# Kernel tuning notes

Measured on AMD Instinct MI355X. Metric: run time of the kernel, lower is better.

Reference implementation:

```python
import jax, jax.numpy as jnp
import numpy as np

N_LEAVES = 256
N_CLASSES = 512
BATCH = 131072


def setup_inputs() -> dict:
    key = jax.random.key(0)
    k1, k2 = jax.random.split(key)
    # opinions: concatenated leaf class distributions [n_leaves, n_classes]
    opinions = jax.random.normal(k1, (N_LEAVES, N_CLASSES), dtype=jnp.float32)
    # weights: concatenated per-leaf path probabilities [batch, n_leaves]
    weights = jax.random.uniform(k2, (BATCH, N_LEAVES), dtype=jnp.float32)
    return {"opinions": opinions, "weights": weights}


def reference(opinions, weights):
    # argmax over leaves per example, then gather that leaf's opinion row.
    # Equivalent to tf: elems = argmax(weights, axis=1); map_fn(lambda x: opinions[x], elems)
    idx = jnp.argmax(weights, axis=1)            # [batch]
    return jnp.take(opinions, idx, axis=0)       # [batch, n_classes]
```

## Files before the change

### kernel.cpp

```cpp
#include <hip/hip_runtime.h>

#define N_LEAVES  256
#define N_CLASSES 512

__global__ __launch_bounds__(256) void OutputLayer_41961830482215_kernel(
    const float* __restrict__ opinions,
    const float* __restrict__ weights,
    float* __restrict__ out,
    int batch)
{
    const int wave = threadIdx.x >> 6;
    const int lane = threadIdx.x & 63;
    const long long row = (long long)blockIdx.x * 4 + wave;
    if (row >= batch) return;

    const float4 w = *reinterpret_cast<const float4*>(weights + row * N_LEAVES + lane * 4);
    float best = w.x;
    int   bidx = lane * 4;
    if (w.y > best) { best = w.y; bidx = lane * 4 + 1; }
    if (w.z > best) { best = w.z; bidx = lane * 4 + 2; }
    if (w.w > best) { best = w.w; bidx = lane * 4 + 3; }

    #pragma unroll
    for (int off = 32; off >= 1; off >>= 1) {
        const float ov = __shfl_xor(best, off);
        const int   oi = __shfl_xor(bidx, off);
        if (ov > best || (ov == best && oi < bidx)) { best = ov; bidx = oi; }
    }

    const float4* __restrict__ src =
        reinterpret_cast<const float4*>(opinions + (long long)bidx * N_CLASSES);
    float4* __restrict__ dst =
        reinterpret_cast<float4*>(out + row * N_CLASSES);
    dst[lane]      = src[lane];
    dst[lane + 64] = src[lane + 64];
}

extern "C" void kernel_launch(void* const* d_in, const int* in_sizes, int n_in,
                              void* d_out, int out_size, void* d_ws, size_t ws_size,
                              hipStream_t stream) {
    const float* opinions = (const float*)d_in[0];
    const float* weights  = (const float*)d_in[1];
    float* out = (float*)d_out;
    const int batch = in_sizes[1] / N_LEAVES;
    const int blocks = (batch + 3) / 4;
    OutputLayer_41961830482215_kernel<<<blocks, 256, 0, stream>>>(
        opinions, weights, out, batch);
}
```

Baseline: 79.18 us.

## Split argmax and gather into two kernels via workspace index buffer

Splits the fused argmax+gather kernel into an argmax kernel that writes per-row indices to the workspace and a gather kernel that copies opinion rows. The fused kernel is kept as a fallback when the workspace is too small. The aim is to separate the read-heavy and write-heavy phases so each streams more cleanly. In exchange it adds a second launch and an extra round trip of the index array through memory.

```diff
diff --git a/kernel.cpp b/kernel.cpp
--- a/kernel.cpp
+++ b/kernel.cpp
@@ -3,10 +3,11 @@
 #define N_LEAVES  256
 #define N_CLASSES 512
 
-__global__ __launch_bounds__(256) void OutputLayer_41961830482215_kernel(
-    const float* __restrict__ opinions,
+typedef float f32x4 __attribute__((ext_vector_type(4)));
+
+__global__ __launch_bounds__(256) void argmax_rows_kernel(
     const float* __restrict__ weights,
-    float* __restrict__ out,
+    int* __restrict__ idx,
     int batch)
 {
     const int wave = threadIdx.x >> 6;
@@ -14,7 +15,7 @@
     const long long row = (long long)blockIdx.x * 4 + wave;
     if (row >= batch) return;
 
-    const float4 w = *reinterpret_cast<const float4*>(weights + row * N_LEAVES + lane * 4);
+    const f32x4 w = *(reinterpret_cast<const f32x4*>(weights + row * N_LEAVES) + lane);
     float best = w.x;
     int   bidx = lane * 4;
     if (w.y > best) { best = w.y; bidx = lane * 4 + 1; }
@@ -27,11 +28,54 @@
         const int   oi = __shfl_xor(bidx, off);
         if (ov > best || (ov == best && oi < bidx)) { best = ov; bidx = oi; }
     }
+    if (lane == 0) idx[row] = bidx;
+}
 
-    const float4* __restrict__ src =
-        reinterpret_cast<const float4*>(opinions + (long long)bidx * N_CLASSES);
-    float4* __restrict__ dst =
-        reinterpret_cast<float4*>(out + row * N_CLASSES);
+__global__ __launch_bounds__(256) void gather_rows_kernel(
+    const float* __restrict__ opinions,
+    const int* __restrict__ idx,
+    float* __restrict__ out,
+    int batch)
+{
+    const int wave = threadIdx.x >> 6;
+    const int lane = threadIdx.x & 63;
+    const long long row = (long long)blockIdx.x * 4 + wave;
+    if (row >= batch) return;
+
+    const int b = idx[row];
+    const f32x4* __restrict__ src =
+        reinterpret_cast<const f32x4*>(opinions + (long long)b * N_CLASSES);
+    f32x4* __restrict__ dst = reinterpret_cast<f32x4*>(out + row * N_CLASSES);
+    dst[lane]      = src[lane];
+    dst[lane + 64] = src[lane + 64];
+}
+
+__global__ __launch_bounds__(256) void fused_kernel(
+    const float* __restrict__ opinions,
+    const float* __restrict__ weights,
+    float* __restrict__ out,
+    int batch)
+{
+    const int wave = threadIdx.x >> 6;
+    const int lane = threadIdx.x & 63;
+    const long long row = (long long)blockIdx.x * 4 + wave;
+    if (row >= batch) return;
+
+    const f32x4 w = *(reinterpret_cast<const f32x4*>(weights + row * N_LEAVES) + lane);
+    float best = w.x;
+    int   bidx = lane * 4;
+    if (w.y > best) { best = w.y; bidx = lane * 4 + 1; }
+    if (w.z > best) { best = w.z; bidx = lane * 4 + 2; }
+    if (w.w > best) { best = w.w; bidx = lane * 4 + 3; }
+    #pragma unroll
+    for (int off = 32; off >= 1; off >>= 1) {
+        const float ov = __shfl_xor(best, off);
+        const int   oi = __shfl_xor(bidx, off);
+        if (ov > best || (ov == best && oi < bidx)) { best = ov; bidx = oi; }
+    }
+    const f32x4* __restrict__ src =
+        reinterpret_cast<const f32x4*>(opinions + (long long)bidx * N_CLASSES);
+    f32x4* __restrict__ dst = reinterpret_cast<f32x4*>(out + row * N_CLASSES);
     dst[lane]      = src[lane];
     dst[lane + 64] = src[lane + 64];
 }
@@ -44,6 +88,12 @@
     float* out = (float*)d_out;
     const int batch = in_sizes[1] / N_LEAVES;
     const int blocks = (batch + 3) / 4;
-    OutputLayer_41961830482215_kernel<<<blocks, 256, 0, stream>>>(
-        opinions, weights, out, batch);
+
+    if (ws_size >= (size_t)batch * sizeof(int)) {
+        int* idx = (int*)d_ws;
+        argmax_rows_kernel<<<blocks, 256, 0, stream>>>(weights, idx, batch);
+        gather_rows_kernel<<<blocks, 256, 0, stream>>>(opinions, idx, out, batch);
+    } else {
+        fused_kernel<<<blocks, 256, 0, stream>>>(opinions, weights, out, batch);
+    }
 }
```

New measurement: 86.89 us. 1.1x slower.

## Use persistent grid-stride loop with next-row prefetch and nontemporal loads/stores

Applied to the files above, without the earlier changes.

Replaces the one-row-per-wave launch with a fixed grid of 2048 blocks. Each wave loops over rows with a grid stride and prefetches the next row's weights before reducing the current one. Weight loads and output stores use nontemporal hints to avoid polluting the cache, while opinion rows stay cached. This aims to hide load latency and cut launch and scheduling overhead. The risk is lower occupancy-driven parallelism on a kernel that is bandwidth-bound.

```diff
diff --git a/kernel.cpp b/kernel.cpp
--- a/kernel.cpp
+++ b/kernel.cpp
@@ -2,6 +2,8 @@
 
 #define N_LEAVES  256
 #define N_CLASSES 512
+
+typedef float f32x4 __attribute__((ext_vector_type(4)));
 
 __global__ __launch_bounds__(256) void OutputLayer_41961830482215_kernel(
     const float* __restrict__ opinions,
@@ -11,29 +13,45 @@
 {
     const int wave = threadIdx.x >> 6;
     const int lane = threadIdx.x & 63;
-    const long long row = (long long)blockIdx.x * 4 + wave;
+    const long long W   = (long long)gridDim.x * 4;
+    const long long gid = (long long)blockIdx.x * 4 + wave;
+
+    long long row = gid;
     if (row >= batch) return;
 
-    const float4 w = *reinterpret_cast<const float4*>(weights + row * N_LEAVES + lane * 4);
-    float best = w.x;
-    int   bidx = lane * 4;
-    if (w.y > best) { best = w.y; bidx = lane * 4 + 1; }
-    if (w.z > best) { best = w.z; bidx = lane * 4 + 2; }
-    if (w.w > best) { best = w.w; bidx = lane * 4 + 3; }
+    f32x4 w_next = __builtin_nontemporal_load(
+        reinterpret_cast<const f32x4*>(weights + row * N_LEAVES) + lane);
 
-    #pragma unroll
-    for (int off = 32; off >= 1; off >>= 1) {
-        const float ov = __shfl_xor(best, off);
-        const int   oi = __shfl_xor(bidx, off);
-        if (ov > best || (ov == best && oi < bidx)) { best = ov; bidx = oi; }
+    while (row < batch) {
+        const f32x4 w = w_next;
+        const long long nrow = row + W;
+        if (nrow < batch) {
+            w_next = __builtin_nontemporal_load(
+                reinterpret_cast<const f32x4*>(weights + nrow * N_LEAVES) + lane);
+        }
+
+        float best = w.x;
+        int   bidx = lane * 4;
+        if (w.y > best) { best = w.y; bidx = lane * 4 + 1; }
+        if (w.z > best) { best = w.z; bidx = lane * 4 + 2; }
+        if (w.w > best) { best = w.w; bidx = lane * 4 + 3; }
+        #pragma unroll
+        for (int off = 32; off >= 1; off >>= 1) {
+            const float ov = __shfl_xor(best, off);
+            const int   oi = __shfl_xor(bidx, off);
+            if (ov > best || (ov == best && oi < bidx)) { best = ov; bidx = oi; }
+        }
+
+        const f32x4* __restrict__ src =
+            reinterpret_cast<const f32x4*>(opinions + (long long)bidx * N_CLASSES);
+        const f32x4 lo = src[lane];
+        const f32x4 hi = src[lane + 64];
+        f32x4* dst = reinterpret_cast<f32x4*>(out + row * N_CLASSES);
+        __builtin_nontemporal_store(lo, dst + lane);
+        __builtin_nontemporal_store(hi, dst + lane + 64);
+
+        row = nrow;
     }
-
-    const float4* __restrict__ src =
-        reinterpret_cast<const float4*>(opinions + (long long)bidx * N_CLASSES);
-    float4* __restrict__ dst =
-        reinterpret_cast<float4*>(out + row * N_CLASSES);
-    dst[lane]      = src[lane];
-    dst[lane + 64] = src[lane + 64];
 }
 
 extern "C" void kernel_launch(void* const* d_in, const int* in_sizes, int n_in,
@@ -43,7 +61,10 @@
     const float* weights  = (const float*)d_in[1];
     float* out = (float*)d_out;
     const int batch = in_sizes[1] / N_LEAVES;
-    const int blocks = (batch + 3) / 4;
+
+    int blocks = 2048;
+    const int max_blocks = (batch + 3) / 4;
+    if (blocks > max_blocks) blocks = max_blocks;
     OutputLayer_41961830482215_kernel<<<blocks, 256, 0, stream>>>(
         opinions, weights, out, batch);
 }
```

New measurement: 84.25 us. 6.4% more time.
